# Performance work log

Measured on AMD Instinct MI355X. Metric: run time of the kernel, lower is better.

Reference implementation:

```python
import jax, jax.numpy as jnp
import numpy as np

B, T, DIM = 2, 2048, 1024
HID = 4096
H, KVH, HD = 16, 4, 64
WIN = 512
NORM_EPS = 1e-5
QK_EPS = 1e-6
LS_INIT = 0.01


def setup_inputs() -> dict:
    key = jax.random.key(0)
    ks = jax.random.split(key, 12)
    s = lambda fan_in: 1.0 / np.sqrt(fan_in)
    return {
        "x": jax.random.normal(ks[0], (B, T, DIM), jnp.float32),
        # torch Linear weights are (out, in); y = x @ W.T
        "wq": jax.random.normal(ks[1], (H * HD, DIM), jnp.float32) * s(DIM),
        "wk": jax.random.normal(ks[2], (KVH * HD, DIM), jnp.float32) * s(DIM),
        "wv": jax.random.normal(ks[3], (KVH * HD, DIM), jnp.float32) * s(DIM),
        "wo": jax.random.normal(ks[4], (DIM, H * HD), jnp.float32) * s(H * HD),
        "w1": jax.random.normal(ks[5], (HID, DIM), jnp.float32) * s(DIM),
        "w2": jax.random.normal(ks[6], (DIM, HID), jnp.float32) * s(HID),
        "w3": jax.random.normal(ks[7], (HID, DIM), jnp.float32) * s(DIM),
        "q_norm_w": jnp.ones((HD,), jnp.float32),
        "k_norm_w": jnp.ones((HD,), jnp.float32),
        "attn_norm_w": jnp.ones((DIM,), jnp.float32),
        "ffn_norm_w": jnp.ones((DIM,), jnp.float32),
        "attn_scale": jnp.full((DIM,), LS_INIT, jnp.float32),
        "ffn_scale": jnp.full((DIM,), LS_INIT, jnp.float32),
    }


def _rmsnorm(x, w, eps):
    return x * jax.lax.rsqrt(jnp.mean(x * x, axis=-1, keepdims=True) + eps) * w


def _attention(x, wq, wk, wv, wo, q_norm_w, k_norm_w):
    b, t, _ = x.shape
    q = (x @ wq.T).reshape(b, t, H, HD)
    k = (x @ wk.T).reshape(b, t, KVH, HD)
    v = (x @ wv.T).reshape(b, t, KVH, HD)
    q = _rmsnorm(q, q_norm_w, QK_EPS)
    k = _rmsnorm(k, k_norm_w, QK_EPS)
    # GQA: repeat kv heads to H heads
    rep = H // KVH
    k = jnp.repeat(k, rep, axis=2)  # (b,t,H,HD)
    v = jnp.repeat(v, rep, axis=2)
    scale = 1.0 / np.sqrt(HD)
    scores = jnp.einsum("bqhd,bkhd->bhqk", q, k) * scale  # (b,H,t,t)
    row = jnp.arange(t)[:, None]
    col = jnp.arange(t)[None, :]
    mask = (row >= col) & (row - col < WIN)  # (t,t) bool
    scores = jnp.where(mask[None, None], scores, -jnp.inf)
    probs = jax.nn.softmax(scores, axis=-1)
    y = jnp.einsum("bhqk,bkhd->bqhd", probs, v).reshape(b, t, H * HD)
    return y @ wo.T


def reference(x, wq, wk, wv, wo, w1, w2, w3, q_norm_w, k_norm_w,
              attn_norm_w, ffn_norm_w, attn_scale, ffn_scale):
    r = _attention(_rmsnorm(x, attn_norm_w, NORM_EPS), wq, wk, wv, wo,
                   q_norm_w, k_norm_w)
    h = x + r * attn_scale
    hn = _rmsnorm(h, ffn_norm_w, NORM_EPS)
    ffn = (jax.nn.silu(hn @ w1.T) * (hn @ w3.T)) @ w2.T
    return h + ffn * ffn_scale
```

## Files before the change

### kernel.cpp

```cpp
#include <hip/hip_runtime.h>

typedef unsigned short u16;
typedef unsigned int u32;
typedef unsigned char u8;
typedef short bf16x8 __attribute__((ext_vector_type(8)));
typedef float f32x4 __attribute__((ext_vector_type(4)));
typedef float f32x16 __attribute__((ext_vector_type(16)));
typedef int i32x4 __attribute__((ext_vector_type(4)));
typedef int i32x8 __attribute__((ext_vector_type(8)));

#define AS1 __attribute__((address_space(1)))
#define AS3 __attribute__((address_space(3)))

#define B_ 2
#define T_ 2048
#define DIM_ 1024
#define HID_ 4096
#define H_ 16
#define KVH_ 4
#define HD_ 64
#define WIN_ 512

#define SCALE_A 0x7C7C7C7C
#define SCALE_B 0x79797979

__device__ __forceinline__ u16 f2bf(float f) {
    union { float f; u32 u; } v; v.f = f;
    u32 r = v.u + 0x7FFFu + ((v.u >> 16) & 1u);
    return (u16)(r >> 16);
}
__device__ __forceinline__ float bf2f(u32 u) {
    union { u32 u; float f; } v; v.u = u << 16;
    return v.f;
}
__device__ __forceinline__ float4 ld4bf(const u16* p) {
    uint2 u = *(const uint2*)p;
    float4 r;
    r.x = bf2f(u.x & 0xFFFFu); r.y = bf2f(u.x >> 16);
    r.z = bf2f(u.y & 0xFFFFu); r.w = bf2f(u.y >> 16);
    return r;
}
__device__ __forceinline__ void load_lds16(const void* g, void* l) {
    __builtin_amdgcn_global_load_lds((AS1 void*)(g), (AS3 void*)(l), 16, 0, 0);
}

__global__ __launch_bounds__(256) void mega_cvt(const float* __restrict__ wq,
                                                const float* __restrict__ wk,
                                                const float* __restrict__ wv,
                                                const float* __restrict__ wo,
                                                const float* __restrict__ w1,
                                                const float* __restrict__ w3,
                                                const float* __restrict__ w2,
                                                u16* __restrict__ wqkv,
                                                u16* __restrict__ wo_b,
                                                u8* __restrict__ w13_8,
                                                u8* __restrict__ w2_8) {
    int i = blockIdx.x * 256 + threadIdx.x;
    if (i < 655360) {
        const float* s; uint2* dbase; size_t didx;
        if (i < 262144)      { s = wq + (size_t)i * 4; dbase = (uint2*)wqkv; didx = i; }
        else if (i < 327680) { int f = i - 262144; s = wk + (size_t)f * 4; dbase = (uint2*)wqkv; didx = 262144 + f; }
        else if (i < 393216) { int f = i - 327680; s = wv + (size_t)f * 4; dbase = (uint2*)wqkv; didx = 327680 + f; }
        else                 { int f = i - 393216; s = wo + (size_t)f * 4; dbase = (uint2*)wo_b; didx = f; }
        float4 v = *(const float4*)s;
        u32 lo = (u32)f2bf(v.x) | ((u32)f2bf(v.y) << 16);
        u32 hi = (u32)f2bf(v.z) | ((u32)f2bf(v.w) << 16);
        dbase[didx] = make_uint2(lo, hi);
    } else {
        const float* s; u32* dbase; size_t didx;
        if (i < 1703936)      { int f = i - 655360;  int c = f >> 8; int n = (c >> 5) * 64 + (c & 31);
                                s = w1 + (size_t)f * 4; dbase = (u32*)w13_8; didx = (size_t)n * 256 + (f & 255); }
        else if (i < 2752512) { int f = i - 1703936; int c = f >> 8; int n = (c >> 5) * 64 + 32 + (c & 31);
                                s = w3 + (size_t)f * 4; dbase = (u32*)w13_8; didx = (size_t)n * 256 + (f & 255); }
        else                  { int f = i - 2752512; s = w2 + (size_t)f * 4; dbase = (u32*)w2_8; didx = f; }
        float4 v = *(const float4*)s;
        int p = __builtin_amdgcn_cvt_pk_fp8_f32(v.x * 64.f, v.y * 64.f, 0, false);
        p = __builtin_amdgcn_cvt_pk_fp8_f32(v.z * 64.f, v.w * 64.f, p, true);
        dbase[didx] = (u32)p;
    }
}

__global__ __launch_bounds__(256) void rmsnorm_kernel(const float* __restrict__ x,
                                                      const float* __restrict__ w,
                                                      u16* __restrict__ out, float eps) {
    int row = blockIdx.x, tid = threadIdx.x;
    const float4 v = ((const float4*)(x + (size_t)row * DIM_))[tid];
    float ss = v.x * v.x + v.y * v.y + v.z * v.z + v.w * v.w;
#pragma unroll
    for (int m = 1; m < 64; m <<= 1) ss += __shfl_xor(ss, m);
    __shared__ float part[4];
    if ((tid & 63) == 0) part[tid >> 6] = ss;
    __syncthreads();
    float tot = part[0] + part[1] + part[2] + part[3];
    float r = rsqrtf(tot * (1.0f / DIM_) + eps);
    const float4 wv = ((const float4*)w)[tid];
    u32 lo = (u32)f2bf(v.x * r * wv.x) | ((u32)f2bf(v.y * r * wv.y) << 16);
    u32 hi = (u32)f2bf(v.z * r * wv.z) | ((u32)f2bf(v.w * r * wv.w) << 16);
    ((uint2*)(out + (size_t)row * DIM_))[tid] = make_uint2(lo, hi);
}

__global__ __launch_bounds__(256) void fuse_attn_kernel(const float* __restrict__ x,
                                                        const u16* __restrict__ p,
                                                        const float* __restrict__ ascale,
                                                        const float* __restrict__ fnw,
                                                        float* __restrict__ h,
                                                        u8* __restrict__ xn8) {
    int row = blockIdx.x, tid = threadIdx.x;
    const float4 xv = ((const float4*)(x + (size_t)row * DIM_))[tid];
    float4 a0 = ld4bf(p + (size_t)row * DIM_ + tid * 4);
    float4 a1 = ld4bf(p + 4194304 + (size_t)row * DIM_ + tid * 4);
    const float4 sc = ((const float4*)ascale)[tid];
    float4 hv;
    hv.x = xv.x + (a0.x + a1.x) * sc.x;
    hv.y = xv.y + (a0.y + a1.y) * sc.y;
    hv.z = xv.z + (a0.z + a1.z) * sc.z;
    hv.w = xv.w + (a0.w + a1.w) * sc.w;
    ((float4*)(h + (size_t)row * DIM_))[tid] = hv;
    float ss = hv.x * hv.x + hv.y * hv.y + hv.z * hv.z + hv.w * hv.w;
#pragma unroll
    for (int m = 1; m < 64; m <<= 1) ss += __shfl_xor(ss, m);
    __shared__ float part[4];
    if ((tid & 63) == 0) part[tid >> 6] = ss;
    __syncthreads();
    float tot = part[0] + part[1] + part[2] + part[3];
    float r = rsqrtf(tot * (1.0f / DIM_) + 1e-5f) * 8.0f;
    const float4 wv = ((const float4*)fnw)[tid];
    int pk = __builtin_amdgcn_cvt_pk_fp8_f32(hv.x * r * wv.x, hv.y * r * wv.y, 0, false);
    pk = __builtin_amdgcn_cvt_pk_fp8_f32(hv.z * r * wv.z, hv.w * r * wv.w, pk, true);
    ((u32*)xn8)[(size_t)row * 256 + tid] = (u32)pk;
}

__global__ __launch_bounds__(256) void fuse_ffn_kernel(const float* __restrict__ h,
                                                       const u16* __restrict__ p,
                                                       const float* __restrict__ fscale,
                                                       float* __restrict__ out) {
    int row = blockIdx.x, tid = threadIdx.x;
    const float4 hv = ((const float4*)(h + (size_t)row * DIM_))[tid];
    size_t off = (size_t)row * DIM_ + tid * 4;
    float4 a0 = ld4bf(p + off);
    float4 a1 = ld4bf(p + 4194304 + off);
    float4 a2 = ld4bf(p + 8388608 + off);
    float4 a3 = ld4bf(p + 12582912 + off);
    const float4 sc = ((const float4*)fscale)[tid];
    float4 o;
    o.x = hv.x + (a0.x + a1.x + a2.x + a3.x) * sc.x;
    o.y = hv.y + (a0.y + a1.y + a2.y + a3.y) * sc.y;
    o.z = hv.z + (a0.z + a1.z + a2.z + a3.z) * sc.z;
    o.w = hv.w + (a0.w + a1.w + a2.w + a3.w) * sc.w;
    ((float4*)(out + (size_t)row * DIM_))[tid] = o;
}

__global__ __launch_bounds__(256) void qkv_post_kernel(const u16* __restrict__ qkv,
                                                       const float* __restrict__ qw,
                                                       const float* __restrict__ kw,
                                                       u16* __restrict__ Qb,
                                                       u16* __restrict__ Kb,
                                                       u16* __restrict__ Vb) {
    int bt = blockIdx.x;
    int b = bt >> 11, t = bt & (T_ - 1);
    int wave = threadIdx.x >> 6, lane = threadIdx.x & 63;
    const u16* row0 = qkv + (size_t)bt * 1536;
    const u16* row1 = row0 + 6291456;
    float qwl = qw[lane], kwl = kw[lane];
#pragma unroll
    for (int i = 0; i < 4; i++) {
        int h = wave * 4 + i;
        float v = bf2f(row0[h * 64 + lane]) + bf2f(row1[h * 64 + lane]);
        float ss = v * v;
#pragma unroll
        for (int m = 1; m < 64; m <<= 1) ss += __shfl_xor(ss, m);
        float r = rsqrtf(ss * (1.0f / 64.0f) + 1e-6f);
        Qb[(((size_t)(b * H_ + h)) * T_ + t) * HD_ + lane] = f2bf(v * r * qwl);
    }
    {
        float v = bf2f(row0[1024 + wave * 64 + lane]) + bf2f(row1[1024 + wave * 64 + lane]);
        float ss = v * v;
#pragma unroll
        for (int m = 1; m < 64; m <<= 1) ss += __shfl_xor(ss, m);
        float r = rsqrtf(ss * (1.0f / 64.0f) + 1e-6f);
        Kb[(((size_t)(b * KVH_ + wave)) * T_ + t) * HD_ + lane] = f2bf(v * r * kwl);
        float vv = bf2f(row0[1280 + wave * 64 + lane]) + bf2f(row1[1280 + wave * 64 + lane]);
        Vb[(((size_t)(b * KVH_ + wave)) * T_ + t) * HD_ + lane] = f2bf(vv);
    }
}

__global__ __launch_bounds__(256) void vtrans_kernel(const u16* __restrict__ Vb,
                                                     u16* __restrict__ Vt) {
    const int bk = blockIdx.x >> 5;
    const int t0 = (blockIdx.x & 31) * 64;
    const int tid = threadIdx.x;
    __shared__ __align__(16) u16 tile[64][64];
    const u16* src = Vb + ((size_t)bk * T_ + t0) * HD_;
#pragma unroll
    for (int i = 0; i < 2; i++) {
        int g = tid + i * 256;
        int r = g >> 3, c8 = g & 7;
        *(bf16x8*)&tile[r][c8 * 8] = *(const bf16x8*)(src + (size_t)r * HD_ + c8 * 8);
    }
    __syncthreads();
    const int d = tid >> 2, ts = (tid & 3) * 16;
    u16 buf[16];
#pragma unroll
    for (int j = 0; j < 16; j++) buf[j] = tile[ts + j][d];
    u16* dst = Vt + (size_t)bk * HD_ * T_ + (size_t)d * T_ + t0 + ts;
    *(bf16x8*)(dst) = *(const bf16x8*)&buf[0];
    *(bf16x8*)(dst + 8) = *(const bf16x8*)&buf[8];
}

__global__ __launch_bounds__(256) void flash_kernel(const u16* __restrict__ Qb,
                                                    const u16* __restrict__ Kb,
                                                    const u16* __restrict__ Vt,
                                                    u16* __restrict__ Ob) {
    const int b = blockIdx.z, h = blockIdx.y, qt = blockIdx.x;
    const int q0 = qt * 64;
    const int tid = threadIdx.x, wave = tid >> 6, lane = tid & 63;
    const int m = lane & 15, quad = lane >> 4;
    const int kvh = h >> 2;

    __shared__ __align__(16) u16 Ps[4][16 * 40];

    const u16* Qp = Qb + ((size_t)(b * H_ + h) * T_) * HD_;
    const u16* Kp = Kb + ((size_t)(b * KVH_ + kvh) * T_) * HD_;
    const u16* Vp = Vt + ((size_t)(b * KVH_ + kvh) * HD_) * T_;

    const int qlo = q0 + wave * 16;
    const int qrow = qlo + m;
    bf16x8 qa0 = *(const bf16x8*)(Qp + (size_t)qrow * 64 + quad * 8);
    bf16x8 qa1 = *(const bf16x8*)(Qp + (size_t)qrow * 64 + 32 + quad * 8);

    f32x4 o0 = {0.f, 0.f, 0.f, 0.f}, o1 = {0.f, 0.f, 0.f, 0.f};
    f32x4 o2 = {0.f, 0.f, 0.f, 0.f}, o3 = {0.f, 0.f, 0.f, 0.f};
    float mrun[4] = {-1e30f, -1e30f, -1e30f, -1e30f};
    float lrun[4] = {0.f, 0.f, 0.f, 0.f};

    const int klo = (qlo - (WIN_ - 1) > 0) ? (qlo - (WIN_ - 1)) : 0;
    const int kt0 = klo >> 5, kt1 = (qlo + 15) >> 5;

    const u16* kp0 = Kp + (size_t)(kt0 * 32 + m) * 64 + quad * 8;
    bf16x8 k00 = *(const bf16x8*)(kp0);
    bf16x8 k01 = *(const bf16x8*)(kp0 + 32);
    bf16x8 k10 = *(const bf16x8*)(kp0 + 16 * 64);
    bf16x8 k11 = *(const bf16x8*)(kp0 + 16 * 64 + 32);

    for (int kt = kt0; kt <= kt1; ++kt) {
        const int kbase = kt << 5;
        f32x4 s0 = {0.f, 0.f, 0.f, 0.f}, s1 = {0.f, 0.f, 0.f, 0.f};
        s0 = __builtin_amdgcn_mfma_f32_16x16x32_bf16(qa0, k00, s0, 0, 0, 0);
        s0 = __builtin_amdgcn_mfma_f32_16x16x32_bf16(qa1, k01, s0, 0, 0, 0);
        s1 = __builtin_amdgcn_mfma_f32_16x16x32_bf16(qa0, k10, s1, 0, 0, 0);
        s1 = __builtin_amdgcn_mfma_f32_16x16x32_bf16(qa1, k11, s1, 0, 0, 0);
        const u16* vp = Vp + (size_t)m * T_ + kbase + quad * 8;
        bf16x8 vb0 = *(const bf16x8*)(vp);
        bf16x8 vb1 = *(const bf16x8*)(vp + 16 * T_);
        bf16x8 vb2 = *(const bf16x8*)(vp + 32 * T_);
        bf16x8 vb3 = *(const bf16x8*)(vp + 48 * T_);
        if (kt < kt1) {
            const u16* kp = Kp + (size_t)(kbase + 32 + m) * 64 + quad * 8;
            k00 = *(const bf16x8*)(kp);
            k01 = *(const bf16x8*)(kp + 32);
            k10 = *(const bf16x8*)(kp + 16 * 64);
            k11 = *(const bf16x8*)(kp + 16 * 64 + 32);
        }
        const bool full = (kbase + 31 <= qlo) && (kbase >= qlo - 496);
#pragma unroll
        for (int r = 0; r < 4; r++) {
            float v0, v1;
            if (full) {
                v0 = s0[r] * 0.125f;
                v1 = s1[r] * 0.125f;
            } else {
                int qg = qlo + quad * 4 + r;
                int kg0 = kbase + m, kg1 = kbase + 16 + m;
                v0 = (kg0 <= qg && qg - kg0 < WIN_) ? s0[r] * 0.125f : -INFINITY;
                v1 = (kg1 <= qg && qg - kg1 < WIN_) ? s1[r] * 0.125f : -INFINITY;
            }
            float rmax = fmaxf(v0, v1);
            rmax = fmaxf(rmax, __shfl_xor(rmax, 1));
            rmax = fmaxf(rmax, __shfl_xor(rmax, 2));
            rmax = fmaxf(rmax, __shfl_xor(rmax, 4));
            rmax = fmaxf(rmax, __shfl_xor(rmax, 8));
            float mnew = fmaxf(mrun[r], rmax);
            float alpha = __expf(mrun[r] - mnew);
            float p0 = __expf(v0 - mnew);
            float p1 = __expf(v1 - mnew);
            float psum = p0 + p1;
            psum += __shfl_xor(psum, 1);
            psum += __shfl_xor(psum, 2);
            psum += __shfl_xor(psum, 4);
            psum += __shfl_xor(psum, 8);
            lrun[r] = lrun[r] * alpha + psum;
            mrun[r] = mnew;
            o0[r] *= alpha; o1[r] *= alpha; o2[r] *= alpha; o3[r] *= alpha;
            Ps[wave][(quad * 4 + r) * 40 + m] = f2bf(p0);
            Ps[wave][(quad * 4 + r) * 40 + 16 + m] = f2bf(p1);
        }
        bf16x8 pa = *(const bf16x8*)&Ps[wave][m * 40 + quad * 8];
        o0 = __builtin_amdgcn_mfma_f32_16x16x32_bf16(pa, vb0, o0, 0, 0, 0);
        o1 = __builtin_amdgcn_mfma_f32_16x16x32_bf16(pa, vb1, o1, 0, 0, 0);
        o2 = __builtin_amdgcn_mfma_f32_16x16x32_bf16(pa, vb2, o2, 0, 0, 0);
        o3 = __builtin_amdgcn_mfma_f32_16x16x32_bf16(pa, vb3, o3, 0, 0, 0);
    }
#pragma unroll
    for (int r = 0; r < 4; r++) {
        int qg = q0 + wave * 16 + quad * 4 + r;
        float inv = 1.0f / lrun[r];
        size_t base = ((size_t)(b * T_ + qg)) * (H_ * HD_) + h * HD_;
        Ob[base + 0 + m] = f2bf(o0[r] * inv);
        Ob[base + 16 + m] = f2bf(o1[r] * inv);
        Ob[base + 32 + m] = f2bf(o2[r] * inv);
        Ob[base + 48 + m] = f2bf(o3[r] * inv);
    }
}

__global__ __launch_bounds__(256) void gemm_bt(const u16* __restrict__ A,
                                               const u16* __restrict__ Bt,
                                               u16* __restrict__ Cb,
                                               int M, int N, int K, int KS) {
    __shared__ __align__(16) u16 As[2][4096];
    __shared__ __align__(16) u16 Bs[2][4096];
    const int tid = threadIdx.x, wave = tid >> 6, lane = tid & 63;
    const int m = lane & 15, quad = lane >> 4;
    const int m0 = blockIdx.y * 128, n0 = blockIdx.x * 128;
    const int wm = (wave >> 1) * 64, wn = (wave & 1) * 64;
    const int kb = blockIdx.z * KS;
    const int nIter = KS >> 5;
    const int slot = wave * 2;
    const int flat0 = slot * 512 + lane * 8;
    const int row0_ = flat0 >> 5, col0 = flat0 & 31;
    const int flat1 = (slot + 1) * 512 + lane * 8;
    const int row1_ = flat1 >> 5, col1 = flat1 & 31;

    f32x4 acc[4][4] = {};

    load_lds16(A + (size_t)(m0 + row0_) * K + kb + col0, &As[0][slot * 512]);
    load_lds16(Bt + (size_t)(n0 + row0_) * K + kb + col0, &Bs[0][slot * 512]);
    load_lds16(A + (size_t)(m0 + row1_) * K + kb + col1, &As[0][(slot + 1) * 512]);
    load_lds16(Bt + (size_t)(n0 + row1_) * K + kb + col1, &Bs[0][(slot + 1) * 512]);

    for (int it = 0; it < nIter; ++it) {
        __syncthreads();
        const int cur = it & 1;
        if (it + 1 < nIter) {
            const int nb = 1 - cur;
            const int k0 = kb + (it + 1) * 32;
            load_lds16(A + (size_t)(m0 + row0_) * K + k0 + col0, &As[nb][slot * 512]);
            load_lds16(Bt + (size_t)(n0 + row0_) * K + k0 + col0, &Bs[nb][slot * 512]);
            load_lds16(A + (size_t)(m0 + row1_) * K + k0 + col1, &As[nb][(slot + 1) * 512]);
            load_lds16(Bt + (size_t)(n0 + row1_) * K + k0 + col1, &Bs[nb][(slot + 1) * 512]);
        }
        bf16x8 af[4], bfr[4];
#pragma unroll
        for (int i = 0; i < 4; i++) af[i] = *(const bf16x8*)&As[cur][(wm + i * 16 + m) * 32 + quad * 8];
#pragma unroll
        for (int j = 0; j < 4; j++) bfr[j] = *(const bf16x8*)&Bs[cur][(wn + j * 16 + m) * 32 + quad * 8];
#pragma unroll
        for (int i = 0; i < 4; i++)
#pragma unroll
            for (int j = 0; j < 4; j++)
                acc[i][j] = __builtin_amdgcn_mfma_f32_16x16x32_bf16(af[i], bfr[j], acc[i][j], 0, 0, 0);
    }

    u16* Cz = Cb + (size_t)blockIdx.z * M * N;
#pragma unroll
    for (int i = 0; i < 4; i++) {
        int rowb = m0 + wm + i * 16 + quad * 4;
#pragma unroll
        for (int j = 0; j < 4; j++) {
            int col = n0 + wn + j * 16 + m;
#pragma unroll
            for (int r = 0; r < 4; r++)
                Cz[(size_t)(rowb + r) * N + col] = f2bf(acc[i][j][r]);
        }
    }
}

#define MFMA8(a, b, c) __builtin_amdgcn_mfma_scale_f32_32x32x64_f8f6f4(a, b, c, 0, 0, 0, SCALE_A, 0, SCALE_B)
#define WAITBAR(N) asm volatile("s_waitcnt vmcnt(" #N ")\n\ts_barrier" ::: "memory")
#define PHASE_MFMA(I0, I1)                           \
    __builtin_amdgcn_s_setprio(1);                   \
    acc[I0][0] = MFMA8(a0, bf0, acc[I0][0]);         \
    acc[I0][1] = MFMA8(a0, bf1, acc[I0][1]);         \
    acc[I1][0] = MFMA8(a1, bf0, acc[I1][0]);         \
    acc[I1][1] = MFMA8(a1, bf1, acc[I1][1]);         \
    __builtin_amdgcn_s_setprio(0);

template <int MODE>
__global__ __launch_bounds__(512) void gemm_fp8(const u8* __restrict__ A,
                                                const u8* __restrict__ Bt,
                                                u16* __restrict__ Cb,
                                                u8* __restrict__ C8,
                                                int M, int N, int K, int KS) {
    __shared__ __align__(16) u8 As[2][32768];
    __shared__ __align__(16) u8 Bs[2][32768];
    const int tid = threadIdx.x, wave = tid >> 6, lane = tid & 63;
    const int l31 = lane & 31, lh = lane >> 5;
    const int m0 = blockIdx.y * 256, n0 = blockIdx.x * 256;
    const int wm = (wave >> 2) * 128, wn = (wave & 3) * 64;
    const int kb = blockIdx.z * KS;
    const int KT = KS >> 7;

    const int srow = ((wave & 3) << 6) + lane;
    const u8* Asrc = A + (size_t)m0 * K + (size_t)srow * K;
    const u8* Bsrc = Bt + (size_t)n0 * K + (size_t)srow * K;
    const int wv2 = wave >> 2;
    const int ldsW = (wave & 3) << 10;

    auto STAGE = [&](const u8* src, int kk, int ks, u8* lds) {
#pragma unroll
        for (int q = 0; q < 2; q++) {
            const int ch = ks * 4 + wv2 + 2 * q;
            load_lds16(src + kk + ch * 16, lds + (ch << 12) + ldsW);
        }
    };
    auto FRAG = [&](const u8* t, int ks, int row) -> i32x8 {
        const int c0 = ks * 4 + (lh << 1);
        union { i32x4 h[2]; i32x8 v; } u;
        u.h[0] = *(const i32x4*)(t + ((c0 << 8) + row) * 16);
        u.h[1] = *(const i32x4*)(t + (((c0 + 1) << 8) + row) * 16);
        return u.v;
    };

    f32x16 acc[4][2] = {};

    STAGE(Asrc, kb, 0, As[0]);
    STAGE(Bsrc, kb, 0, Bs[0]);
    STAGE(Asrc, kb, 1, As[0]);
    STAGE(Bsrc, kb, 1, Bs[0]);

    for (int kt = 0; kt < KT - 1; ++kt) {
        const int cur = kt & 1, nb = cur ^ 1;
        const u8* Ac = As[cur];
        const u8* Bc = Bs[cur];
        const int kn = kb + (kt + 1) * 128;
        i32x8 bf0, bf1, a0, a1;
        STAGE(Asrc, kn, 0, As[nb]);
        WAITBAR(6);
        bf0 = FRAG(Bc, 0, wn + l31);
        bf1 = FRAG(Bc, 0, wn + 32 + l31);
        a0 = FRAG(Ac, 0, wm + l31);
        a1 = FRAG(Ac, 0, wm + 32 + l31);
        PHASE_MFMA(0, 1)
        STAGE(Bsrc, kn, 0, Bs[nb]);
        a0 = FRAG(Ac, 0, wm + 64 + l31);
        a1 = FRAG(Ac, 0, wm + 96 + l31);
        PHASE_MFMA(2, 3)
        STAGE(Asrc, kn, 1, As[nb]);
        WAITBAR(6);
        bf0 = FRAG(Bc, 1, wn + l31);
        bf1 = FRAG(Bc, 1, wn + 32 + l31);
        a0 = FRAG(Ac, 1, wm + l31);
        a1 = FRAG(Ac, 1, wm + 32 + l31);
        PHASE_MFMA(0, 1)
        STAGE(Bsrc, kn, 1, Bs[nb]);
        a0 = FRAG(Ac, 1, wm + 64 + l31);
        a1 = FRAG(Ac, 1, wm + 96 + l31);
        PHASE_MFMA(2, 3)
    }
    {
        const int cur = (KT - 1) & 1;
        const u8* Ac = As[cur];
        const u8* Bc = Bs[cur];
        i32x8 bf0, bf1, a0, a1;
        WAITBAR(4);
        bf0 = FRAG(Bc, 0, wn + l31);
        bf1 = FRAG(Bc, 0, wn + 32 + l31);
        a0 = FRAG(Ac, 0, wm + l31);
        a1 = FRAG(Ac, 0, wm + 32 + l31);
        PHASE_MFMA(0, 1)
        a0 = FRAG(Ac, 0, wm + 64 + l31);
        a1 = FRAG(Ac, 0, wm + 96 + l31);
        PHASE_MFMA(2, 3)
        WAITBAR(0);
        bf0 = FRAG(Bc, 1, wn + l31);
        bf1 = FRAG(Bc, 1, wn + 32 + l31);
        a0 = FRAG(Ac, 1, wm + l31);
        a1 = FRAG(Ac, 1, wm + 32 + l31);
        PHASE_MFMA(0, 1)
        a0 = FRAG(Ac, 1, wm + 64 + l31);
        a1 = FRAG(Ac, 1, wm + 96 + l31);
        PHASE_MFMA(2, 3)
    }

    if (MODE == 0) {
        u16* Cz = Cb + (size_t)blockIdx.z * M * N;
#pragma unroll
        for (int i = 0; i < 4; i++)
#pragma unroll
            for (int j = 0; j < 2; j++) {
                int col = n0 + wn + j * 32 + l31;
#pragma unroll
                for (int reg = 0; reg < 16; reg++) {
                    int row = m0 + wm + i * 32 + (reg & 3) + 8 * (reg >> 2) + 4 * lh;
                    Cz[(size_t)row * N + col] = f2bf(acc[i][j][reg]);
                }
            }
    } else {
        int c = (n0 >> 1) + (wn >> 1) + l31;
#pragma unroll
        for (int i = 0; i < 4; i++)
#pragma unroll
            for (int reg = 0; reg < 16; reg++) {
                int row = m0 + wm + i * 32 + (reg & 3) + 8 * (reg >> 2) + 4 * lh;
                float g1 = acc[i][0][reg], g3 = acc[i][1][reg];
                float res = (g1 / (1.f + __expf(-g1))) * g3 * 8.0f;
                int p = __builtin_amdgcn_cvt_pk_fp8_f32(res, res, 0, false);
                C8[(size_t)row * (N >> 1) + c] = (u8)(p & 0xFF);
            }
    }
}

extern "C" void kernel_launch(void* const* d_in, const int* in_sizes, int n_in,
                              void* d_out, int out_size, void* d_ws, size_t ws_size,
                              hipStream_t stream) {
    const float* x = (const float*)d_in[0];
    const float* wq = (const float*)d_in[1];
    const float* wk = (const float*)d_in[2];
    const float* wv = (const float*)d_in[3];
    const float* wo = (const float*)d_in[4];
    const float* w1 = (const float*)d_in[5];
    const float* w2 = (const float*)d_in[6];
    const float* w3 = (const float*)d_in[7];
    const float* qnw = (const float*)d_in[8];
    const float* knw = (const float*)d_in[9];
    const float* anw = (const float*)d_in[10];
    const float* fnw = (const float*)d_in[11];
    const float* ascale = (const float*)d_in[12];
    const float* fscale = (const float*)d_in[13];
    float* out = (float*)d_out;

    char* ws = (char*)d_ws;
    u16* wqkv_bf = (u16*)(ws + 0);
    u16* wo_bf = (u16*)(ws + 3145728);
    u8* w13_8 = (u8*)(ws + 5242880);
    u8* w2_8 = (u8*)(ws + 13631488);
    u16* xn_bf = (u16*)(ws + 17825792);
    u8* xn8 = (u8*)(ws + 26214400);
    float* h_f = (float*)(ws + 30408704);
    char* P = ws + 47185920;
    u16* qkv_part = (u16*)(P + 0);
    u16* Qb = (u16*)(P + 25165824);
    u16* Kb = (u16*)(P + 33554432);
    u16* Vb = (u16*)(P + 35651584);
    u16* att_bf = (u16*)(P + 37748736);
    u16* Vt = (u16*)(P + 46137344);
    u16* wo_part = (u16*)(P + 0);
    u8* gsw8 = (u8*)(P + 16777216);
    u16* w2_part = (u16*)(P + 33554432);

    mega_cvt<<<14848, 256, 0, stream>>>(wq, wk, wv, wo, w1, w3, w2,
                                        wqkv_bf, wo_bf, w13_8, w2_8);
    rmsnorm_kernel<<<4096, 256, 0, stream>>>(x, anw, xn_bf, 1e-5f);
    gemm_bt<<<dim3(12, 32, 2), 256, 0, stream>>>(xn_bf, wqkv_bf, qkv_part,
                                                 4096, 1536, 1024, 512);
    qkv_post_kernel<<<4096, 256, 0, stream>>>(qkv_part, qnw, knw, Qb, Kb, Vb);
    vtrans_kernel<<<256, 256, 0, stream>>>(Vb, Vt);
    flash_kernel<<<dim3(32, 16, 2), 256, 0, stream>>>(Qb, Kb, Vt, att_bf);
    gemm_bt<<<dim3(8, 32, 2), 256, 0, stream>>>(att_bf, wo_bf, wo_part,
                                                4096, 1024, 1024, 512);
    fuse_attn_kernel<<<4096, 256, 0, stream>>>(x, wo_part, ascale, fnw, h_f, xn8);
    gemm_fp8<1><<<dim3(32, 16, 1), 512, 0, stream>>>(xn8, w13_8, nullptr, gsw8,
                                                     4096, 8192, 1024, 1024);
    gemm_fp8<0><<<dim3(4, 16, 4), 512, 0, stream>>>(gsw8, w2_8, w2_part, nullptr,
                                                    4096, 1024, 4096, 1024);
    fuse_ffn_kernel<<<4096, 256, 0, stream>>>(h_f, w2_part, fscale, out);
}
```

Before: 355.8 us.

## Split flash attention KV range across two wave halves with LDS combine

Doubles the flash attention block to 512 threads. Each group of four waves now handles the same 16-row query slices over half of the sliding-window KV tiles. The upper half writes its partial O, running max and running sum to shared memory, and the lower half merges them with a log-sum-exp rescale before writing the output. This shortens each wave's serial KV loop and adds parallelism to a latency-bound kernel. The cost is extra LDS use, a block barrier, and duplicated Q loads.

```diff
diff --git a/kernel.cpp b/kernel.cpp
--- a/kernel.cpp
+++ b/kernel.cpp
@@ -207,23 +207,26 @@
     *(bf16x8*)(dst + 8) = *(const bf16x8*)&buf[8];
 }
 
-__global__ __launch_bounds__(256) void flash_kernel(const u16* __restrict__ Qb,
-                                                    const u16* __restrict__ Kb,
-                                                    const u16* __restrict__ Vt,
-                                                    u16* __restrict__ Ob) {
+__global__ __launch_bounds__(512, 8) void flash_kernel(const u16* __restrict__ Qb,
+                                                       const u16* __restrict__ Kb,
+                                                       const u16* __restrict__ Vt,
+                                                       u16* __restrict__ Ob) {
     const int b = blockIdx.z, h = blockIdx.y, qt = blockIdx.x;
     const int q0 = qt * 64;
     const int tid = threadIdx.x, wave = tid >> 6, lane = tid & 63;
+    const int qw = wave & 3, half = wave >> 2;
     const int m = lane & 15, quad = lane >> 4;
     const int kvh = h >> 2;
 
-    __shared__ __align__(16) u16 Ps[4][16 * 40];
+    __shared__ __align__(16) u16 Ps[8][16 * 40];
+    __shared__ __align__(16) float CombO[4][64][16];
+    __shared__ float CombML[4][64][8];
 
     const u16* Qp = Qb + ((size_t)(b * H_ + h) * T_) * HD_;
     const u16* Kp = Kb + ((size_t)(b * KVH_ + kvh) * T_) * HD_;
     const u16* Vp = Vt + ((size_t)(b * KVH_ + kvh) * HD_) * T_;
 
-    const int qlo = q0 + wave * 16;
+    const int qlo = q0 + qw * 16;
     const int qrow = qlo + m;
     bf16x8 qa0 = *(const bf16x8*)(Qp + (size_t)qrow * 64 + quad * 8);
     bf16x8 qa1 = *(const bf16x8*)(Qp + (size_t)qrow * 64 + 32 + quad * 8);
@@ -235,14 +238,17 @@
 
     const int klo = (qlo - (WIN_ - 1) > 0) ? (qlo - (WIN_ - 1)) : 0;
     const int kt0 = klo >> 5, kt1 = (qlo + 15) >> 5;
-
-    const u16* kp0 = Kp + (size_t)(kt0 * 32 + m) * 64 + quad * 8;
+    const int nLo = (kt1 - kt0 + 1) >> 1;
+    const int myKt0 = half ? (kt0 + nLo) : kt0;
+    const int myKt1 = half ? kt1 : (kt0 + nLo - 1);
+
+    const u16* kp0 = Kp + (size_t)(myKt0 * 32 + m) * 64 + quad * 8;
     bf16x8 k00 = *(const bf16x8*)(kp0);
     bf16x8 k01 = *(const bf16x8*)(kp0 + 32);
     bf16x8 k10 = *(const bf16x8*)(kp0 + 16 * 64);
     bf16x8 k11 = *(const bf16x8*)(kp0 + 16 * 64 + 32);
 
-    for (int kt = kt0; kt <= kt1; ++kt) {
+    for (int kt = myKt0; kt <= myKt1; ++kt) {
         const int kbase = kt << 5;
         f32x4 s0 = {0.f, 0.f, 0.f, 0.f}, s1 = {0.f, 0.f, 0.f, 0.f};
         s0 = __builtin_amdgcn_mfma_f32_16x16x32_bf16(qa0, k00, s0, 0, 0, 0);
@@ -254,7 +260,7 @@
         bf16x8 vb1 = *(const bf16x8*)(vp + 16 * T_);
         bf16x8 vb2 = *(const bf16x8*)(vp + 32 * T_);
         bf16x8 vb3 = *(const bf16x8*)(vp + 48 * T_);
-        if (kt < kt1) {
+        if (kt < myKt1) {
             const u16* kp = Kp + (size_t)(kbase + 32 + m) * 64 + quad * 8;
             k00 = *(const bf16x8*)(kp);
             k01 = *(const bf16x8*)(kp + 32);
@@ -300,15 +306,40 @@
         o2 = __builtin_amdgcn_mfma_f32_16x16x32_bf16(pa, vb2, o2, 0, 0, 0);
         o3 = __builtin_amdgcn_mfma_f32_16x16x32_bf16(pa, vb3, o3, 0, 0, 0);
     }
-#pragma unroll
-    for (int r = 0; r < 4; r++) {
-        int qg = q0 + wave * 16 + quad * 4 + r;
-        float inv = 1.0f / lrun[r];
-        size_t base = ((size_t)(b * T_ + qg)) * (H_ * HD_) + h * HD_;
-        Ob[base + 0 + m] = f2bf(o0[r] * inv);
-        Ob[base + 16 + m] = f2bf(o1[r] * inv);
-        Ob[base + 32 + m] = f2bf(o2[r] * inv);
-        Ob[base + 48 + m] = f2bf(o3[r] * inv);
+
+    if (half) {
+        float* co = &CombO[qw][lane][0];
+        *(f32x4*)(co + 0) = o0;
+        *(f32x4*)(co + 4) = o1;
+        *(f32x4*)(co + 8) = o2;
+        *(f32x4*)(co + 12) = o3;
+        float* cm = &CombML[qw][lane][0];
+        cm[0] = mrun[0]; cm[1] = mrun[1]; cm[2] = mrun[2]; cm[3] = mrun[3];
+        cm[4] = lrun[0]; cm[5] = lrun[1]; cm[6] = lrun[2]; cm[7] = lrun[3];
+    }
+    __syncthreads();
+    if (!half) {
+        const float* co = &CombO[qw][lane][0];
+        const float* cm = &CombML[qw][lane][0];
+        f32x4 u0 = *(const f32x4*)(co + 0);
+        f32x4 u1 = *(const f32x4*)(co + 4);
+        f32x4 u2 = *(const f32x4*)(co + 8);
+        f32x4 u3 = *(const f32x4*)(co + 12);
+#pragma unroll
+        for (int r = 0; r < 4; r++) {
+            float m1 = cm[r], l1 = cm[4 + r];
+            float mf = fmaxf(mrun[r], m1);
+            float a0 = __expf(mrun[r] - mf);
+            float a1 = __expf(m1 - mf);
+            float inv = 1.0f / (lrun[r] * a0 + l1 * a1);
+            float b0 = a0 * inv, b1 = a1 * inv;
+            int qg = qlo + quad * 4 + r;
+            size_t base = ((size_t)(b * T_ + qg)) * (H_ * HD_) + h * HD_;
+            Ob[base + 0 + m]  = f2bf(o0[r] * b0 + u0[r] * b1);
+            Ob[base + 16 + m] = f2bf(o1[r] * b0 + u1[r] * b1);
+            Ob[base + 32 + m] = f2bf(o2[r] * b0 + u2[r] * b1);
+            Ob[base + 48 + m] = f2bf(o3[r] * b0 + u3[r] * b1);
+        }
     }
 }
 
@@ -554,7 +585,7 @@
                                                  4096, 1536, 1024, 512);
     qkv_post_kernel<<<4096, 256, 0, stream>>>(qkv_part, qnw, knw, Qb, Kb, Vb);
     vtrans_kernel<<<256, 256, 0, stream>>>(Vb, Vt);
-    flash_kernel<<<dim3(32, 16, 2), 256, 0, stream>>>(Qb, Kb, Vt, att_bf);
+    flash_kernel<<<dim3(32, 16, 2), 512, 0, stream>>>(Qb, Kb, Vt, att_bf);
     gemm_bt<<<dim3(8, 32, 2), 256, 0, stream>>>(att_bf, wo_bf, wo_part,
                                                 4096, 1024, 1024, 512);
     fuse_attn_kernel<<<4096, 256, 0, stream>>>(x, wo_part, ascale, fnw, h_f, xn8);
```

Measured after the change: 475.6 us. +33.7%, slower.

## Transpose flash attention MFMA layout and widen KV tile to 64

Applied to the files above, without the earlier changes.

The flash attention kernel now computes S^T = K·Q^T so each lane owns one query row. Row max and sum reductions then need only two cross-lane shuffles instead of four per row. The KV step widens from 32 to 64 keys per iteration, and P is written to LDS and O to global memory as packed vectors. This cuts shuffle and exp bookkeeping overhead per key, at the cost of more registers for K/V fragments and 16 scores per lane.

```diff
diff --git a/kernel.cpp b/kernel.cpp
--- a/kernel.cpp
+++ b/kernel.cpp
@@ -217,7 +217,7 @@
     const int m = lane & 15, quad = lane >> 4;
     const int kvh = h >> 2;
 
-    __shared__ __align__(16) u16 Ps[4][16 * 40];
+    __shared__ __align__(16) u16 Ps[4][16 * 72];
 
     const u16* Qp = Qb + ((size_t)(b * H_ + h) * T_) * HD_;
     const u16* Kp = Kb + ((size_t)(b * KVH_ + kvh) * T_) * HD_;
@@ -228,87 +228,104 @@
     bf16x8 qa0 = *(const bf16x8*)(Qp + (size_t)qrow * 64 + quad * 8);
     bf16x8 qa1 = *(const bf16x8*)(Qp + (size_t)qrow * 64 + 32 + quad * 8);
 
-    f32x4 o0 = {0.f, 0.f, 0.f, 0.f}, o1 = {0.f, 0.f, 0.f, 0.f};
-    f32x4 o2 = {0.f, 0.f, 0.f, 0.f}, o3 = {0.f, 0.f, 0.f, 0.f};
-    float mrun[4] = {-1e30f, -1e30f, -1e30f, -1e30f};
-    float lrun[4] = {0.f, 0.f, 0.f, 0.f};
-
-    const int klo = (qlo - (WIN_ - 1) > 0) ? (qlo - (WIN_ - 1)) : 0;
-    const int kt0 = klo >> 5, kt1 = (qlo + 15) >> 5;
-
-    const u16* kp0 = Kp + (size_t)(kt0 * 32 + m) * 64 + quad * 8;
-    bf16x8 k00 = *(const bf16x8*)(kp0);
-    bf16x8 k01 = *(const bf16x8*)(kp0 + 32);
-    bf16x8 k10 = *(const bf16x8*)(kp0 + 16 * 64);
-    bf16x8 k11 = *(const bf16x8*)(kp0 + 16 * 64 + 32);
+    f32x4 o[4] = {};
+    float mrun = -1e30f, lrun = 0.f;
+
+    const int kt0 = (qlo >= WIN_) ? ((qlo - (WIN_ - 1)) >> 6) : 0;
+    const int kt1 = (qlo + 15) >> 6;
+
+    bf16x8 kf[4][2];
+#pragma unroll
+    for (int st = 0; st < 4; st++) {
+        const u16* kp = Kp + (size_t)(kt0 * 64 + st * 16 + m) * 64 + quad * 8;
+        kf[st][0] = *(const bf16x8*)(kp);
+        kf[st][1] = *(const bf16x8*)(kp + 32);
+    }
 
     for (int kt = kt0; kt <= kt1; ++kt) {
-        const int kbase = kt << 5;
-        f32x4 s0 = {0.f, 0.f, 0.f, 0.f}, s1 = {0.f, 0.f, 0.f, 0.f};
-        s0 = __builtin_amdgcn_mfma_f32_16x16x32_bf16(qa0, k00, s0, 0, 0, 0);
-        s0 = __builtin_amdgcn_mfma_f32_16x16x32_bf16(qa1, k01, s0, 0, 0, 0);
-        s1 = __builtin_amdgcn_mfma_f32_16x16x32_bf16(qa0, k10, s1, 0, 0, 0);
-        s1 = __builtin_amdgcn_mfma_f32_16x16x32_bf16(qa1, k11, s1, 0, 0, 0);
-        const u16* vp = Vp + (size_t)m * T_ + kbase + quad * 8;
-        bf16x8 vb0 = *(const bf16x8*)(vp);
-        bf16x8 vb1 = *(const bf16x8*)(vp + 16 * T_);
-        bf16x8 vb2 = *(const bf16x8*)(vp + 32 * T_);
-        bf16x8 vb3 = *(const bf16x8*)(vp + 48 * T_);
+        const int kbase = kt << 6;
+        f32x4 s[4];
+#pragma unroll
+        for (int st = 0; st < 4; st++) {
+            f32x4 z = {0.f, 0.f, 0.f, 0.f};
+            z = __builtin_amdgcn_mfma_f32_16x16x32_bf16(kf[st][0], qa0, z, 0, 0, 0);
+            z = __builtin_amdgcn_mfma_f32_16x16x32_bf16(kf[st][1], qa1, z, 0, 0, 0);
+            s[st] = z;
+        }
+        bf16x8 vb[4][2];
+#pragma unroll
+        for (int d = 0; d < 4; d++) {
+            const u16* vp = Vp + (size_t)(d * 16 + m) * T_ + kbase + quad * 8;
+            vb[d][0] = *(const bf16x8*)(vp);
+            vb[d][1] = *(const bf16x8*)(vp + 32);
+        }
         if (kt < kt1) {
-            const u16* kp = Kp + (size_t)(kbase + 32 + m) * 64 + quad * 8;
-            k00 = *(const bf16x8*)(kp);
-            k01 = *(const bf16x8*)(kp + 32);
-            k10 = *(const bf16x8*)(kp + 16 * 64);
-            k11 = *(const bf16x8*)(kp + 16 * 64 + 32);
-        }
-        const bool full = (kbase + 31 <= qlo) && (kbase >= qlo - 496);
-#pragma unroll
-        for (int r = 0; r < 4; r++) {
-            float v0, v1;
-            if (full) {
-                v0 = s0[r] * 0.125f;
-                v1 = s1[r] * 0.125f;
-            } else {
-                int qg = qlo + quad * 4 + r;
-                int kg0 = kbase + m, kg1 = kbase + 16 + m;
-                v0 = (kg0 <= qg && qg - kg0 < WIN_) ? s0[r] * 0.125f : -INFINITY;
-                v1 = (kg1 <= qg && qg - kg1 < WIN_) ? s1[r] * 0.125f : -INFINITY;
+#pragma unroll
+            for (int st = 0; st < 4; st++) {
+                const u16* kp = Kp + (size_t)(kbase + 64 + st * 16 + m) * 64 + quad * 8;
+                kf[st][0] = *(const bf16x8*)(kp);
+                kf[st][1] = *(const bf16x8*)(kp + 32);
             }
-            float rmax = fmaxf(v0, v1);
-            rmax = fmaxf(rmax, __shfl_xor(rmax, 1));
-            rmax = fmaxf(rmax, __shfl_xor(rmax, 2));
-            rmax = fmaxf(rmax, __shfl_xor(rmax, 4));
-            rmax = fmaxf(rmax, __shfl_xor(rmax, 8));
-            float mnew = fmaxf(mrun[r], rmax);
-            float alpha = __expf(mrun[r] - mnew);
-            float p0 = __expf(v0 - mnew);
-            float p1 = __expf(v1 - mnew);
-            float psum = p0 + p1;
-            psum += __shfl_xor(psum, 1);
-            psum += __shfl_xor(psum, 2);
-            psum += __shfl_xor(psum, 4);
-            psum += __shfl_xor(psum, 8);
-            lrun[r] = lrun[r] * alpha + psum;
-            mrun[r] = mnew;
-            o0[r] *= alpha; o1[r] *= alpha; o2[r] *= alpha; o3[r] *= alpha;
-            Ps[wave][(quad * 4 + r) * 40 + m] = f2bf(p0);
-            Ps[wave][(quad * 4 + r) * 40 + 16 + m] = f2bf(p1);
-        }
-        bf16x8 pa = *(const bf16x8*)&Ps[wave][m * 40 + quad * 8];
-        o0 = __builtin_amdgcn_mfma_f32_16x16x32_bf16(pa, vb0, o0, 0, 0, 0);
-        o1 = __builtin_amdgcn_mfma_f32_16x16x32_bf16(pa, vb1, o1, 0, 0, 0);
-        o2 = __builtin_amdgcn_mfma_f32_16x16x32_bf16(pa, vb2, o2, 0, 0, 0);
-        o3 = __builtin_amdgcn_mfma_f32_16x16x32_bf16(pa, vb3, o3, 0, 0, 0);
-    }
-#pragma unroll
-    for (int r = 0; r < 4; r++) {
-        int qg = q0 + wave * 16 + quad * 4 + r;
-        float inv = 1.0f / lrun[r];
-        size_t base = ((size_t)(b * T_ + qg)) * (H_ * HD_) + h * HD_;
-        Ob[base + 0 + m] = f2bf(o0[r] * inv);
-        Ob[base + 16 + m] = f2bf(o1[r] * inv);
-        Ob[base + 32 + m] = f2bf(o2[r] * inv);
-        Ob[base + 48 + m] = f2bf(o3[r] * inv);
+        }
+        float v[16];
+        const bool full = (kbase + 63 <= qlo) && (kbase >= qlo - (WIN_ - 16));
+        if (full) {
+#pragma unroll
+            for (int i = 0; i < 16; i++) v[i] = s[i >> 2][i & 3] * 0.125f;
+        } else {
+            const int D = qrow - kbase - quad * 4;
+#pragma unroll
+            for (int st = 0; st < 4; st++)
+#pragma unroll
+                for (int r = 0; r < 4; r++) {
+                    int diff = D - st * 16 - r;
+                    v[st * 4 + r] = ((u32)diff < (u32)WIN_) ? s[st][r] * 0.125f : -INFINITY;
+                }
+        }
+        float t0 = fmaxf(fmaxf(fmaxf(v[0], v[1]), fmaxf(v[2], v[3])),
+                         fmaxf(fmaxf(v[4], v[5]), fmaxf(v[6], v[7])));
+        float t1 = fmaxf(fmaxf(fmaxf(v[8], v[9]), fmaxf(v[10], v[11])),
+                         fmaxf(fmaxf(v[12], v[13]), fmaxf(v[14], v[15])));
+        float rmax = fmaxf(t0, t1);
+        rmax = fmaxf(rmax, __shfl_xor(rmax, 16));
+        rmax = fmaxf(rmax, __shfl_xor(rmax, 32));
+        float mnew = fmaxf(mrun, rmax);
+        float alpha = __expf(mrun - mnew);
+        float p[16];
+#pragma unroll
+        for (int i = 0; i < 16; i++) p[i] = __expf(v[i] - mnew);
+        float u0 = ((p[0] + p[1]) + (p[2] + p[3])) + ((p[4] + p[5]) + (p[6] + p[7]));
+        float u1 = ((p[8] + p[9]) + (p[10] + p[11])) + ((p[12] + p[13]) + (p[14] + p[15]));
+        float psum = u0 + u1;
+        psum += __shfl_xor(psum, 16);
+        psum += __shfl_xor(psum, 32);
+        lrun = lrun * alpha + psum;
+        mrun = mnew;
+#pragma unroll
+        for (int d = 0; d < 4; d++) {
+            o[d][0] *= alpha; o[d][1] *= alpha; o[d][2] *= alpha; o[d][3] *= alpha;
+        }
+#pragma unroll
+        for (int st = 0; st < 4; st++) {
+            u32 lo = (u32)f2bf(p[st * 4 + 0]) | ((u32)f2bf(p[st * 4 + 1]) << 16);
+            u32 hi = (u32)f2bf(p[st * 4 + 2]) | ((u32)f2bf(p[st * 4 + 3]) << 16);
+            *(uint2*)&Ps[wave][m * 72 + st * 16 + quad * 4] = make_uint2(lo, hi);
+        }
+        bf16x8 pa0 = *(const bf16x8*)&Ps[wave][m * 72 + quad * 8];
+        bf16x8 pa1 = *(const bf16x8*)&Ps[wave][m * 72 + 32 + quad * 8];
+#pragma unroll
+        for (int d = 0; d < 4; d++) {
+            o[d] = __builtin_amdgcn_mfma_f32_16x16x32_bf16(vb[d][0], pa0, o[d], 0, 0, 0);
+            o[d] = __builtin_amdgcn_mfma_f32_16x16x32_bf16(vb[d][1], pa1, o[d], 0, 0, 0);
+        }
+    }
+    float inv = 1.0f / lrun;
+    u16* ob = Ob + ((size_t)(b * T_ + qrow)) * (H_ * HD_) + h * HD_;
+#pragma unroll
+    for (int d = 0; d < 4; d++) {
+        u32 lo = (u32)f2bf(o[d][0] * inv) | ((u32)f2bf(o[d][1] * inv) << 16);
+        u32 hi = (u32)f2bf(o[d][2] * inv) | ((u32)f2bf(o[d][3] * inv) << 16);
+        *(uint2*)(ob + d * 16 + quad * 4) = make_uint2(lo, hi);
     }
 }
 
```

Measured after the change: 355.7 us. No clear change (-0.0%).
